# Kernel tuning notes

Measured on AMD Instinct MI355X. Metric: run time of the kernel, lower is better.

Reference implementation:

```python
import jax, jax.numpy as jnp
import numpy as np

N_NODES = 100000
N_EDGES = 1000000
IN_CH = 312
HID = 256
OUT = 256


def _sage_conv(x, src, dst, W_l, b_l, W_r, num_nodes):
    # PyG SAGEConv (mean aggr): out = mean_{j in N(i)} x_j @ W_l + b_l + x_i @ W_r
    msg = x[src]                                             # [E, C] gather
    agg = jax.ops.segment_sum(msg, dst, num_segments=num_nodes)  # [N, C]
    deg = jax.ops.segment_sum(jnp.ones((src.shape[0],), dtype=x.dtype), dst,
                              num_segments=num_nodes)        # [N]
    mean = agg / jnp.maximum(deg, 1.0)[:, None]
    return mean @ W_l + b_l + x @ W_r


def setup_inputs() -> dict:
    key = jax.random.key(0)
    ks = jax.random.split(key, 8)
    x = jax.random.normal(ks[0], (N_NODES, IN_CH), dtype=jnp.float32)
    edge_index = jax.random.randint(ks[1], (2, N_EDGES), 0, N_NODES, dtype=jnp.int64)
    s1 = 1.0 / np.sqrt(IN_CH)
    s2 = 1.0 / np.sqrt(HID)
    W1_l = jax.random.normal(ks[2], (IN_CH, HID), dtype=jnp.float32) * s1
    b1 = jnp.zeros((HID,), dtype=jnp.float32)
    W1_r = jax.random.normal(ks[3], (IN_CH, HID), dtype=jnp.float32) * s1
    W2_l = jax.random.normal(ks[4], (HID, OUT), dtype=jnp.float32) * s2
    b2 = jnp.zeros((OUT,), dtype=jnp.float32)
    W2_r = jax.random.normal(ks[5], (HID, OUT), dtype=jnp.float32) * s2
    return {"x": x, "edge_index": edge_index, "W1_l": W1_l, "b1": b1,
            "W1_r": W1_r, "W2_l": W2_l, "b2": b2, "W2_r": W2_r}


def reference(x, edge_index, W1_l, b1, W1_r, W2_l, b2, W2_r):
    src, dst = edge_index[0], edge_index[1]
    n = x.shape[0]
    h = _sage_conv(x, src, dst, W1_l, b1, W1_r, n)
    h = jax.nn.relu(h)
    out = _sage_conv(h, src, dst, W2_l, b2, W2_r, n)
    return out
```

## Files before the change

kernel.cpp:

```cpp
#include <hip/hip_runtime.h>
#include <hip/hip_bf16.h>
#include <cstdint>
#include <cstddef>

#define IN_CH 312
#define HID 256

typedef __attribute__((ext_vector_type(8))) short bf16x8;
typedef __attribute__((ext_vector_type(4))) float f32x4;
typedef __attribute__((ext_vector_type(8))) unsigned short ushort8;

__device__ __forceinline__ unsigned short f2bf(float f) {
    union { float f; unsigned u; } v; v.f = f;
    const unsigned r = v.u + 0x7FFFu + ((v.u >> 16) & 1u);
    return (unsigned short)(r >> 16);
}
__device__ __forceinline__ float bf2f(unsigned short s) {
    union { unsigned u; float f; } v; v.u = (unsigned)s << 16;
    return v.f;
}
__device__ __forceinline__ void gload_lds16(const void* g, void* l) {
    __builtin_amdgcn_global_load_lds(
        (const __attribute__((address_space(1))) void*)g,
        (__attribute__((address_space(3))) void*)l, 16, 0, 0);
}

__global__ void detect_idx_kernel(const void* __restrict__ ei, int* __restrict__ flag) {
    if (blockIdx.x == 0 && threadIdx.x == 0) {
        const int* p = (const int*)ei;
        int ok = 1;
        for (int i = 0; i < 64; ++i) ok &= (p[2 * i + 1] == 0);
        *flag = ok;
    }
}
__device__ __forceinline__ long long load_idx(const void* ei, long long i, bool is64) {
    return is64 ? ((const long long*)ei)[i] : (long long)((const int*)ei)[i];
}

__global__ void hist_kernel(const void* __restrict__ ei, const int* __restrict__ flag,
                            int* __restrict__ cnt, int E) {
    const int i = blockIdx.x * blockDim.x + threadIdx.x;
    if (i >= E) return;
    const bool is64 = (*flag != 0);
    atomicAdd(&cnt[load_idx(ei, (long long)E + i, is64)], 1);
}

__global__ void offsets_kernel(const int* __restrict__ cnt, int* __restrict__ counter,
                               int* __restrict__ beg, int* __restrict__ cur, int n) {
    const int i = blockIdx.x * blockDim.x + threadIdx.x;
    if (i >= n) return;
    const int b = atomicAdd(counter, cnt[i]);
    beg[i] = b;
    cur[i] = b;
}

__global__ void fill_kernel(const void* __restrict__ ei, const int* __restrict__ flag,
                            int* __restrict__ cur, int* __restrict__ col, int E) {
    const int i = blockIdx.x * blockDim.x + threadIdx.x;
    if (i >= E) return;
    const bool is64 = (*flag != 0);
    const long long s = load_idx(ei, i, is64);
    const long long d = load_idx(ei, (long long)E + i, is64);
    col[atomicAdd(&cur[d], 1)] = (int)s;
}

__global__ void convert_w_kernel(const float* __restrict__ Wl, const float* __restrict__ Wr,
                                 unsigned short* __restrict__ wt, int K, int Kpad) {
    const int tid = blockIdx.x * blockDim.x + threadIdx.x;
    if (tid >= 512 * Kpad) return;
    const int c = tid / Kpad;
    const int k = tid % Kpad;
    float v = 0.f;
    if (k < K) v = (c < 256) ? Wl[(size_t)k * 256 + c] : Wr[(size_t)k * 256 + (c - 256)];
    wt[(size_t)c * Kpad + k] = f2bf(v);
}

template <int KPAD, bool AFP32, bool ZBF16>
__global__ __launch_bounds__(512) void mfma_gemm_kernel(
    const void* __restrict__ Avoid,
    const unsigned short* __restrict__ WT,
    const float* __restrict__ bias,
    unsigned short* __restrict__ Y,
    void* __restrict__ Z,
    int M)
{
    constexpr int NS = KPAD / 32;
    __shared__ __align__(16) char smem[49152];

    const int tid  = (int)threadIdx.x;
    const int lane = tid & 63;
    const int wid  = tid >> 6;
    const int wr = wid >> 1, wc = wid & 1;
    const int r0 = blockIdx.x * 128;
    const int c0 = blockIdx.y * 256;

    const int lrow = lane & 15;
    const int kgrp = lane >> 4;

    f32x4 acc[2][8];
    #pragma unroll
    for (int i = 0; i < 2; ++i)
        #pragma unroll
        for (int j = 0; j < 8; ++j) acc[i][j] = (f32x4)0.f;

    const int glrow = lane >> 2;
    const int glc   = (lane & 3) ^ ((glrow >> 1) & 3);

    const int srow = tid >> 2;
    const int sc   = tid & 3;
    const int sgr  = min(r0 + srow, M - 1);
    const int swbyte = srow * 64 + ((sc ^ ((srow >> 1) & 3)) * 16);

    auto stageB = [&](int t, int b) {
        char* bb = smem + 16384 + b * 16384;
        const int kb = t * 32;
        #pragma unroll
        for (int j = 0; j < 2; ++j) {
            const int ld = wid * 2 + j;
            const int row = ld * 16 + glrow;
            gload_lds16(WT + (size_t)(c0 + row) * KPAD + kb + glc * 8,
                        bb + ld * 1024);
        }
    };
    auto stageA_g = [&](int t, int b) {
        char* ab = smem + b * 8192;
        const unsigned short* A = (const unsigned short*)Avoid;
        const int row = wid * 16 + glrow;
        const int gr = min(r0 + row, M - 1);
        gload_lds16(A + (size_t)gr * KPAD + t * 32 + glc * 8, ab + wid * 1024);
    };
    float4 va, vb;
    auto loadA_r = [&](int t) {
        const float* A = (const float*)Avoid;
        const int gk = t * 32 + sc * 8;
        if (gk < IN_CH) {
            va = *(const float4*)(A + (size_t)sgr * IN_CH + gk);
            vb = *(const float4*)(A + (size_t)sgr * IN_CH + gk + 4);
        } else {
            va = make_float4(0.f, 0.f, 0.f, 0.f);
            vb = make_float4(0.f, 0.f, 0.f, 0.f);
        }
    };
    auto writeA = [&](int b) {
        ushort8 o;
        o[0] = f2bf(va.x); o[1] = f2bf(va.y); o[2] = f2bf(va.z); o[3] = f2bf(va.w);
        o[4] = f2bf(vb.x); o[5] = f2bf(vb.y); o[6] = f2bf(vb.z); o[7] = f2bf(vb.w);
        *(ushort8*)(smem + b * 8192 + swbyte) = o;
    };
    auto compute = [&](int b) {
        const char* ab = smem + b * 8192;
        const char* bb = smem + 16384 + b * 16384;
        bf16x8 af[2], bg[8];
        #pragma unroll
        for (int f = 0; f < 2; ++f) {
            const int arow = wr * 32 + f * 16 + lrow;
            const int p = kgrp ^ ((arow >> 1) & 3);
            af[f] = *(const bf16x8*)(ab + arow * 64 + p * 16);
        }
        #pragma unroll
        for (int fn = 0; fn < 8; ++fn) {
            const int brow = wc * 128 + fn * 16 + lrow;
            const int p = kgrp ^ ((brow >> 1) & 3);
            bg[fn] = *(const bf16x8*)(bb + brow * 64 + p * 16);
        }
        #pragma unroll
        for (int fn = 0; fn < 8; ++fn) {
            acc[0][fn] = __builtin_amdgcn_mfma_f32_16x16x32_bf16(af[0], bg[fn], acc[0][fn], 0, 0, 0);
            acc[1][fn] = __builtin_amdgcn_mfma_f32_16x16x32_bf16(af[1], bg[fn], acc[1][fn], 0, 0, 0);
        }
    };

    stageB(0, 0);
    if (AFP32) { loadA_r(0); writeA(0); }
    else       { stageA_g(0, 0); }
    __syncthreads();

    for (int t = 0; t < NS; ++t) {
        const int b = t & 1, nb = b ^ 1;
        if (t + 1 < NS) {
            stageB(t + 1, nb);
            if (AFP32) loadA_r(t + 1);
            else       stageA_g(t + 1, nb);
        }
        compute(b);
        if (AFP32 && t + 1 < NS) writeA(nb);
        __syncthreads();
    }

    const bool isY = (c0 == 0);
    const int cloc = wc * 128 + (lane & 15);

    if (isY || ZBF16) {
        constexpr int CST = 264;
        short* c_lds = (short*)smem;
        float bv4[8];
        #pragma unroll
        for (int fn = 0; fn < 8; ++fn)
            bv4[fn] = isY ? 0.f : bias[cloc + fn * 16];
        #pragma unroll
        for (int h = 0; h < 2; ++h) {
            __syncthreads();
            if ((wr >> 1) == h) {
                const int lr0 = (wr & 1) * 32 + (lane >> 4) * 4;
                #pragma unroll
                for (int fm = 0; fm < 2; ++fm)
                    #pragma unroll
                    for (int fn = 0; fn < 8; ++fn)
                        #pragma unroll
                        for (int r = 0; r < 4; ++r)
                            c_lds[(lr0 + fm * 16 + r) * CST + cloc + fn * 16] =
                                (short)f2bf(acc[fm][fn][r] + bv4[fn]);
            }
            __syncthreads();
            const int row = tid >> 3;
            const int cb  = (tid & 7) * 32;
            const int gr  = r0 + h * 64 + row;
            if (gr < M) {
                unsigned short* dst = isY
                    ? (Y + (size_t)gr * 256 + cb)
                    : ((unsigned short*)Z + (size_t)gr * 256 + cb);
                #pragma unroll
                for (int j = 0; j < 4; ++j)
                    *(ushort8*)(dst + j * 8) =
                        *(const ushort8*)&c_lds[row * CST + cb + j * 8];
            }
        }
    } else {
        constexpr int CSTF = 264;
        float* cf = (float*)smem;
        float bvf[8];
        #pragma unroll
        for (int fn = 0; fn < 8; ++fn) bvf[fn] = bias[cloc + fn * 16];
        #pragma unroll
        for (int qp = 0; qp < 4; ++qp) {
            __syncthreads();
            if (wr == qp) {
                const int lr0 = (lane >> 4) * 4;
                #pragma unroll
                for (int fm = 0; fm < 2; ++fm)
                    #pragma unroll
                    for (int fn = 0; fn < 8; ++fn)
                        #pragma unroll
                        for (int r = 0; r < 4; ++r)
                            cf[(fm * 16 + lr0 + r) * CSTF + cloc + fn * 16] =
                                acc[fm][fn][r] + bvf[fn];
            }
            __syncthreads();
            const int row = tid >> 4;
            const int cb  = (tid & 15) * 16;
            const int gr  = r0 + qp * 32 + row;
            if (gr < M) {
                float* dst = (float*)Z + (size_t)gr * 256 + cb;
                #pragma unroll
                for (int j = 0; j < 4; ++j)
                    *(float4*)(dst + j * 4) = *(const float4*)&cf[row * CSTF + cb + j * 4];
            }
        }
    }
}

template <bool LAYER1>
__global__ void gather_agg_kernel(const unsigned short* __restrict__ Y,
                                  const int* __restrict__ beg_arr,
                                  const int* __restrict__ cnt,
                                  const int* __restrict__ col,
                                  const void* __restrict__ Z,
                                  void* __restrict__ OUT, int N)
{
    const long long gw = ((long long)blockIdx.x * blockDim.x + threadIdx.x) >> 6;
    if (gw >= N) return;
    const int w = (int)gw;
    const int lane = threadIdx.x & 63;
    const int c4 = lane * 4;
    const int beg = beg_arr[w];
    const int deg = cnt[w];
    const int end = beg + deg;

    float4 a0 = make_float4(0.f, 0.f, 0.f, 0.f);
    float4 a1 = make_float4(0.f, 0.f, 0.f, 0.f);
    int e = beg;
    for (; e + 3 < end; e += 4) {
        const int s0 = col[e], s1 = col[e + 1], s2 = col[e + 2], s3 = col[e + 3];
        const ushort4 v0 = *(const ushort4*)(Y + (size_t)s0 * 256 + c4);
        const ushort4 v1 = *(const ushort4*)(Y + (size_t)s1 * 256 + c4);
        const ushort4 v2 = *(const ushort4*)(Y + (size_t)s2 * 256 + c4);
        const ushort4 v3 = *(const ushort4*)(Y + (size_t)s3 * 256 + c4);
        a0.x += bf2f(v0.x) + bf2f(v1.x);  a1.x += bf2f(v2.x) + bf2f(v3.x);
        a0.y += bf2f(v0.y) + bf2f(v1.y);  a1.y += bf2f(v2.y) + bf2f(v3.y);
        a0.z += bf2f(v0.z) + bf2f(v1.z);  a1.z += bf2f(v2.z) + bf2f(v3.z);
        a0.w += bf2f(v0.w) + bf2f(v1.w);  a1.w += bf2f(v2.w) + bf2f(v3.w);
    }
    for (; e < end; ++e) {
        const ushort4 v0 = *(const ushort4*)(Y + (size_t)col[e] * 256 + c4);
        a0.x += bf2f(v0.x); a0.y += bf2f(v0.y);
        a0.z += bf2f(v0.z); a0.w += bf2f(v0.w);
    }
    float4 acc;
    acc.x = a0.x + a1.x; acc.y = a0.y + a1.y;
    acc.z = a0.z + a1.z; acc.w = a0.w + a1.w;

    const float inv = 1.0f / fmaxf((float)deg, 1.0f);
    float4 z;
    if (LAYER1) {
        const ushort4 zb = *(const ushort4*)((const unsigned short*)Z + (size_t)w * 256 + c4);
        z = make_float4(bf2f(zb.x), bf2f(zb.y), bf2f(zb.z), bf2f(zb.w));
    } else {
        z = *(const float4*)((const float*)Z + (size_t)w * 256 + c4);
    }
    float4 o;
    o.x = acc.x * inv + z.x;
    o.y = acc.y * inv + z.y;
    o.z = acc.z * inv + z.z;
    o.w = acc.w * inv + z.w;
    if (LAYER1) {
        o.x = fmaxf(o.x, 0.f); o.y = fmaxf(o.y, 0.f);
        o.z = fmaxf(o.z, 0.f); o.w = fmaxf(o.w, 0.f);
        ushort4 ob;
        ob.x = f2bf(o.x); ob.y = f2bf(o.y); ob.z = f2bf(o.z); ob.w = f2bf(o.w);
        *(ushort4*)((unsigned short*)OUT + (size_t)w * 256 + c4) = ob;
    } else {
        *(float4*)((float*)OUT + (size_t)w * 256 + c4) = o;
    }
}

extern "C" void kernel_launch(void* const* d_in, const int* in_sizes, int n_in,
                              void* d_out, int out_size, void* d_ws, size_t ws_size,
                              hipStream_t stream) {
    const float* x   = (const float*)d_in[0];
    const void*  ei  = d_in[1];
    const float* W1l = (const float*)d_in[2];
    const float* b1  = (const float*)d_in[3];
    const float* W1r = (const float*)d_in[4];
    const float* W2l = (const float*)d_in[5];
    const float* b2  = (const float*)d_in[6];
    const float* W2r = (const float*)d_in[7];

    const int N = in_sizes[0] / IN_CH;
    const int E = in_sizes[1] / 2;

    char* ws = (char*)d_ws;
    size_t off = 0;
    auto alloc = [&](size_t bytes) {
        void* p = ws + off;
        off = (off + bytes + 255) & ~(size_t)255;
        return p;
    };
    int* flag    = (int*)alloc(4);
    int* cnt     = (int*)alloc((size_t)(N + 1) * 4);
    int* counter = cnt + N;
    int* beg     = (int*)alloc((size_t)N * 4);
    int* cur     = (int*)alloc((size_t)N * 4);
    int* col     = (int*)alloc((size_t)E * 4);
    unsigned short* wt1 = (unsigned short*)alloc((size_t)512 * 320 * 2);
    unsigned short* wt2 = (unsigned short*)alloc((size_t)512 * 256 * 2);
    unsigned short* hb  = (unsigned short*)alloc((size_t)N * 256 * 2);
    unsigned short* y   = (unsigned short*)alloc((size_t)N * 256 * 2);

    float* out = (float*)d_out;
    unsigned short* z1 = (unsigned short*)d_out;

    hipMemsetAsync(cnt, 0, (size_t)(N + 1) * 4, stream);
    detect_idx_kernel<<<1, 64, 0, stream>>>(ei, flag);
    hist_kernel<<<(E + 255) / 256, 256, 0, stream>>>(ei, flag, cnt, E);
    offsets_kernel<<<(N + 255) / 256, 256, 0, stream>>>(cnt, counter, beg, cur, N);
    fill_kernel<<<(E + 255) / 256, 256, 0, stream>>>(ei, flag, cur, col, E);

    convert_w_kernel<<<(512 * 320 + 255) / 256, 256, 0, stream>>>(W1l, W1r, wt1, IN_CH, 320);
    convert_w_kernel<<<(512 * 256 + 255) / 256, 256, 0, stream>>>(W2l, W2r, wt2, HID, 256);

    const dim3 ggrid((N + 127) / 128, 2);

    mfma_gemm_kernel<320, true, true><<<ggrid, 512, 0, stream>>>(x, wt1, b1, y, z1, N);
    gather_agg_kernel<true><<<(N + 3) / 4, 256, 0, stream>>>(y, beg, cnt, col, z1, hb, N);

    mfma_gemm_kernel<256, false, false><<<ggrid, 512, 0, stream>>>(hb, wt2, b2, y, out, N);
    gather_agg_kernel<false><<<(N + 3) / 4, 256, 0, stream>>>(y, beg, cnt, col, out, out, N);
}
```

Measured before the change: 496.3 us.

## Pre-convert x to bf16 and pipeline GEMM loads two stages ahead

Adds a separate kernel that converts x to padded bf16 once, so the first GEMM can stage A directly into LDS with async global-to-LDS loads instead of converting fp32 in registers per tile. The GEMM main loop now issues loads two k-steps ahead and uses explicit vmcnt waits and barriers instead of __syncthreads, aiming to overlap memory with MFMA. The bf16 x buffer is reused for the hidden activations. It adds an extra kernel launch and a full pass over x, and relies on hand-written waitcnt counts matching the number of loads per stage.

```diff
diff --git a/kernel.cpp b/kernel.cpp
--- a/kernel.cpp
+++ b/kernel.cpp
@@ -62,6 +62,24 @@
     const long long s = load_idx(ei, i, is64);
     const long long d = load_idx(ei, (long long)E + i, is64);
     col[atomicAdd(&cur[d], 1)] = (int)s;
+}
+
+__global__ void convert_x_kernel(const float* __restrict__ x, unsigned short* __restrict__ xb,
+                                 int N) {
+    const int tid = blockIdx.x * blockDim.x + threadIdx.x;
+    if (tid >= N * 40) return;
+    const int row = tid / 40;
+    const int c8 = (tid % 40) * 8;
+    ushort8 o;
+    if (c8 < IN_CH) {
+        const float4 v0 = *(const float4*)(x + (size_t)row * IN_CH + c8);
+        const float4 v1 = *(const float4*)(x + (size_t)row * IN_CH + c8 + 4);
+        o[0] = f2bf(v0.x); o[1] = f2bf(v0.y); o[2] = f2bf(v0.z); o[3] = f2bf(v0.w);
+        o[4] = f2bf(v1.x); o[5] = f2bf(v1.y); o[6] = f2bf(v1.z); o[7] = f2bf(v1.w);
+    } else {
+        o = (ushort8)0;
+    }
+    *(ushort8*)(xb + (size_t)row * 320 + c8) = o;
 }
 
 __global__ void convert_w_kernel(const float* __restrict__ Wl, const float* __restrict__ Wr,
@@ -75,9 +93,9 @@
     wt[(size_t)c * Kpad + k] = f2bf(v);
 }
 
-template <int KPAD, bool AFP32, bool ZBF16>
+template <int KPAD, bool ZBF16>
 __global__ __launch_bounds__(512) void mfma_gemm_kernel(
-    const void* __restrict__ Avoid,
+    const unsigned short* __restrict__ A,
     const unsigned short* __restrict__ WT,
     const float* __restrict__ bias,
     unsigned short* __restrict__ Y,
@@ -106,12 +124,8 @@
     const int glrow = lane >> 2;
     const int glc   = (lane & 3) ^ ((glrow >> 1) & 3);
 
-    const int srow = tid >> 2;
-    const int sc   = tid & 3;
-    const int sgr  = min(r0 + srow, M - 1);
-    const int swbyte = srow * 64 + ((sc ^ ((srow >> 1) & 3)) * 16);
-
-    auto stageB = [&](int t, int b) {
+    auto stage = [&](int t, int b) {
+        char* ab = smem + b * 8192;
         char* bb = smem + 16384 + b * 16384;
         const int kb = t * 32;
         #pragma unroll
@@ -121,31 +135,9 @@
             gload_lds16(WT + (size_t)(c0 + row) * KPAD + kb + glc * 8,
                         bb + ld * 1024);
         }
-    };
-    auto stageA_g = [&](int t, int b) {
-        char* ab = smem + b * 8192;
-        const unsigned short* A = (const unsigned short*)Avoid;
-        const int row = wid * 16 + glrow;
-        const int gr = min(r0 + row, M - 1);
-        gload_lds16(A + (size_t)gr * KPAD + t * 32 + glc * 8, ab + wid * 1024);
-    };
-    float4 va, vb;
-    auto loadA_r = [&](int t) {
-        const float* A = (const float*)Avoid;
-        const int gk = t * 32 + sc * 8;
-        if (gk < IN_CH) {
-            va = *(const float4*)(A + (size_t)sgr * IN_CH + gk);
-            vb = *(const float4*)(A + (size_t)sgr * IN_CH + gk + 4);
-        } else {
-            va = make_float4(0.f, 0.f, 0.f, 0.f);
-            vb = make_float4(0.f, 0.f, 0.f, 0.f);
-        }
-    };
-    auto writeA = [&](int b) {
-        ushort8 o;
-        o[0] = f2bf(va.x); o[1] = f2bf(va.y); o[2] = f2bf(va.z); o[3] = f2bf(va.w);
-        o[4] = f2bf(vb.x); o[5] = f2bf(vb.y); o[6] = f2bf(vb.z); o[7] = f2bf(vb.w);
-        *(ushort8*)(smem + b * 8192 + swbyte) = o;
+        const int arow = wid * 16 + glrow;
+        const int gr = min(r0 + arow, M - 1);
+        gload_lds16(A + (size_t)gr * KPAD + kb + glc * 8, ab + wid * 1024);
     };
     auto compute = [&](int b) {
         const char* ab = smem + b * 8192;
@@ -170,21 +162,24 @@
         }
     };
 
-    stageB(0, 0);
-    if (AFP32) { loadA_r(0); writeA(0); }
-    else       { stageA_g(0, 0); }
-    __syncthreads();
-
+    stage(0, 0);
+    stage(1, 1);
+
+    #pragma unroll
     for (int t = 0; t < NS; ++t) {
-        const int b = t & 1, nb = b ^ 1;
+        const int b = t & 1;
         if (t + 1 < NS) {
-            stageB(t + 1, nb);
-            if (AFP32) loadA_r(t + 1);
-            else       stageA_g(t + 1, nb);
-        }
+            asm volatile("s_waitcnt vmcnt(3)" ::: "memory");
+        } else {
+            asm volatile("s_waitcnt vmcnt(0)" ::: "memory");
+        }
+        asm volatile("s_barrier" ::: "memory");
+        __builtin_amdgcn_sched_barrier(0);
         compute(b);
-        if (AFP32 && t + 1 < NS) writeA(nb);
-        __syncthreads();
+        if (t + 2 < NS) {
+            asm volatile("s_barrier" ::: "memory");
+            stage(t + 2, b);
+        }
     }
 
     const bool isY = (c0 == 0);
@@ -353,8 +348,10 @@
     int* col     = (int*)alloc((size_t)E * 4);
     unsigned short* wt1 = (unsigned short*)alloc((size_t)512 * 320 * 2);
     unsigned short* wt2 = (unsigned short*)alloc((size_t)512 * 256 * 2);
-    unsigned short* hb  = (unsigned short*)alloc((size_t)N * 256 * 2);
+    unsigned short* xb  = (unsigned short*)alloc((size_t)N * 320 * 2);
     unsigned short* y   = (unsigned short*)alloc((size_t)N * 256 * 2);
+
+    unsigned short* hb = xb;
 
     float* out = (float*)d_out;
     unsigned short* z1 = (unsigned short*)d_out;
@@ -365,14 +362,15 @@
     offsets_kernel<<<(N + 255) / 256, 256, 0, stream>>>(cnt, counter, beg, cur, N);
     fill_kernel<<<(E + 255) / 256, 256, 0, stream>>>(ei, flag, cur, col, E);
 
+    convert_x_kernel<<<(N * 40 + 255) / 256, 256, 0, stream>>>(x, xb, N);
     convert_w_kernel<<<(512 * 320 + 255) / 256, 256, 0, stream>>>(W1l, W1r, wt1, IN_CH, 320);
     convert_w_kernel<<<(512 * 256 + 255) / 256, 256, 0, stream>>>(W2l, W2r, wt2, HID, 256);
 
     const dim3 ggrid((N + 127) / 128, 2);
 
-    mfma_gemm_kernel<320, true, true><<<ggrid, 512, 0, stream>>>(x, wt1, b1, y, z1, N);
+    mfma_gemm_kernel<320, true><<<ggrid, 512, 0, stream>>>(xb, wt1, b1, y, z1, N);
     gather_agg_kernel<true><<<(N + 3) / 4, 256, 0, stream>>>(y, beg, cnt, col, z1, hb, N);
 
-    mfma_gemm_kernel<256, false, false><<<ggrid, 512, 0, stream>>>(hb, wt2, b2, y, out, N);
+    mfma_gemm_kernel<256, false><<<ggrid, 512, 0, stream>>>(hb, wt2, b2, y, out, N);
     gather_agg_kernel<false><<<(N + 3) / 4, 256, 0, stream>>>(y, beg, cnt, col, out, out, N);
 }
```

Measured after the change: 494.1 us. About the same (-0.4%).
